# Kernel tuning notes

Measured on AMD Instinct MI355X. Metric: run time of the kernel, lower is better.

## Reference

```python
import jax, jax.numpy as jnp
import numpy as np

D_MODEL = 768
N_HEADS = 4
N_POINTS = 4
PATCH = 16
IMG = 224
HF = IMG // PATCH  # 14
WF = IMG // PATCH  # 14
LQ = HF * WF       # 196 tokens
DH = D_MODEL // N_HEADS  # 192


def setup_inputs() -> dict:
    key = jax.random.key(0)
    ks = jax.random.split(key, 14)
    s = 0.02
    inp = {
        "x": jax.random.normal(ks[0], (4, 16, 3, IMG, IMG), dtype=jnp.float32),
        # patch-embed conv (Conv2d 3->768, k=16, s=16)
        "embed_w": s * jax.random.normal(ks[1], (D_MODEL, 3, PATCH, PATCH), dtype=jnp.float32),
        "embed_b": jnp.zeros((D_MODEL,), dtype=jnp.float32),
        # MSDeformAttn linears (nn.Linear stores W as [out, in]; y = x @ W.T + b)
        "value_w": s * jax.random.normal(ks[2], (D_MODEL, D_MODEL), dtype=jnp.float32),
        "value_b": jnp.zeros((D_MODEL,), dtype=jnp.float32),
        "off_w": s * jax.random.normal(ks[3], (N_HEADS * N_POINTS * 2, D_MODEL), dtype=jnp.float32),
        "off_b": s * jax.random.normal(ks[4], (N_HEADS * N_POINTS * 2,), dtype=jnp.float32),
        "aw_w": s * jax.random.normal(ks[5], (N_HEADS * N_POINTS, D_MODEL), dtype=jnp.float32),
        "aw_b": jnp.zeros((N_HEADS * N_POINTS,), dtype=jnp.float32),
        "outp_w": s * jax.random.normal(ks[6], (D_MODEL, D_MODEL), dtype=jnp.float32),
        "outp_b": jnp.zeros((D_MODEL,), dtype=jnp.float32),
        # final nn.Linear proj
        "proj_w": s * jax.random.normal(ks[7], (D_MODEL, D_MODEL), dtype=jnp.float32),
        "proj_b": jnp.zeros((D_MODEL,), dtype=jnp.float32),
    }
    return inp


def _patch_embed(x, w, b):
    # x: (N,3,H,W); non-overlapping 16x16 patches == Conv2d(3,D,16,16)
    N = x.shape[0]
    xh = x.reshape(N, 3, HF, PATCH, WF, PATCH)
    feat = jnp.einsum('nchpwq,dcpq->nhwd', xh, w) + b  # (N,HF,WF,D)
    return feat.reshape(N, LQ, D_MODEL)


def _ref_points():
    lin = jnp.linspace(0.0, 1.0, HF)
    gy, gx = jnp.meshgrid(lin, lin, indexing='ij')
    return jnp.stack([gx, gy], -1).reshape(LQ, 2)  # (Lq, 2) in [0,1], (x,y)


def _deform_attn_core(value, loc, attn):
    # value: (N, Lq, M, Dh); loc: (N, Lq, M, P, 2) normalized [0,1]; attn: (N, Lq, M, P)
    N = value.shape[0]
    # grid_sample align_corners=False: pixel = (2*loc-1 + 1)*S/2 - 0.5 = loc*S - 0.5
    px = loc[..., 0] * WF - 0.5
    py = loc[..., 1] * HF - 0.5
    x0 = jnp.floor(px).astype(jnp.int32)
    y0 = jnp.floor(py).astype(jnp.int32)
    x1, y1 = x0 + 1, y0 + 1
    wx1 = px - x0.astype(px.dtype)
    wy1 = py - y0.astype(py.dtype)
    wx0, wy0 = 1.0 - wx1, 1.0 - wy1

    valh = value.transpose(0, 2, 1, 3)  # (N, M, HW, Dh)

    def gather(ix, iy):
        valid = (ix >= 0) & (ix < WF) & (iy >= 0) & (iy < HF)  # zeros padding
        idx = jnp.clip(iy, 0, HF - 1) * WF + jnp.clip(ix, 0, WF - 1)
        idxm = idx.transpose(0, 2, 1, 3).reshape(N, N_HEADS, LQ * N_POINTS)
        g = jnp.take_along_axis(valh, idxm[..., None], axis=2)  # (N,M,Lq*P,Dh)
        g = g * valid.transpose(0, 2, 1, 3).reshape(N, N_HEADS, LQ * N_POINTS, 1)
        return g.reshape(N, N_HEADS, LQ, N_POINTS, DH)

    def w4(a, b):  # (N,Lq,M,P) -> (N,M,Lq,P,1)
        return (a * b).transpose(0, 2, 1, 3)[..., None]

    sampled = (w4(wx0, wy0) * gather(x0, y0) + w4(wx1, wy0) * gather(x1, y0)
               + w4(wx0, wy1) * gather(x0, y1) + w4(wx1, wy1) * gather(x1, y1))
    # weighted combine over points
    out = (sampled * attn.transpose(0, 2, 1, 3)[..., None]).sum(3)  # (N,M,Lq,Dh)
    return out.transpose(0, 2, 1, 3).reshape(N, LQ, D_MODEL)


def reference(x, embed_w, embed_b, value_w, value_b, off_w, off_b, aw_w, aw_b,
              outp_w, outp_b, proj_w, proj_b):
    B, T = x.shape[0], x.shape[1]
    N = B * T
    xi = x.reshape(N, 3, IMG, IMG)
    feat = _patch_embed(xi, embed_w, embed_b)  # (N, Lq, D)

    # MSDeformAttn (n_levels=1)
    value = (feat @ value_w.T + value_b).reshape(N, LQ, N_HEADS, DH)
    off = (feat @ off_w.T + off_b).reshape(N, LQ, N_HEADS, N_POINTS, 2)
    aw = (feat @ aw_w.T + aw_b).reshape(N, LQ, N_HEADS, N_POINTS)
    aw = jax.nn.softmax(aw, axis=-1)  # softmax over n_levels*n_points = 4

    ref = _ref_points()  # (Lq, 2)
    norm = jnp.array([WF, HF], dtype=feat.dtype)  # offset_normalizer = (W, H)
    loc = ref[None, :, None, None, :] + off / norm  # (N,Lq,M,P,2)

    out = _deform_attn_core(value, loc, aw)
    out = out @ outp_w.T + outp_b  # output_proj

    pooled = out.mean(axis=1)  # mean over tokens
    final = pooled @ proj_w.T + proj_b
    return final.reshape(B, T, D_MODEL)
```

## Files before the change

kernel.cpp:

```cpp
#include <hip/hip_runtime.h>
#include <hip/hip_bf16.h>


using bf16 = __bf16;
typedef bf16  bf16x8 __attribute__((ext_vector_type(8)));
typedef float f32x4  __attribute__((ext_vector_type(4)));

#define N_IMG   64
#define LQ      196
#define DM      768
#define NH      4
#define DH      192
#define M_ROWS  (N_IMG * LQ)
#define NCAT    896

#define OFF_A      ((size_t)0)
#define OFF_WEMBT  (OFF_A     + 19267584)
#define OFF_WCAT   (OFF_WEMBT + 1179648)
#define OFF_WFUSE  (OFF_WCAT  + 1376256)
#define OFF_BFUSE  (OFF_WFUSE + 1376256)
#define OFF_ZB     (OFF_BFUSE + 4096)
#define OFF_VBUF   (OFF_ZB    + 4096)
#define OFF_OA     (OFF_VBUF  + 19267584)
#define OFF_CORE   (OFF_OA    + 3211264)
#define OFF_POOL   (OFF_CORE  + 196608)

__device__ __forceinline__ void gload_lds16(const bf16* g, bf16* l) {
#if __has_builtin(__builtin_amdgcn_global_load_lds)
  __builtin_amdgcn_global_load_lds(
      (const __attribute__((address_space(1))) void*)g,
      (__attribute__((address_space(3))) void*)l, 16, 0, 0);
#else
  *(bf16x8*)l = *(const bf16x8*)g;
#endif
}

__global__ void stage_kernel(const float* __restrict__ x,
                             const float* __restrict__ embed_w,
                             const float* __restrict__ embed_b,
                             const float* __restrict__ value_w,
                             const float* __restrict__ off_w,
                             const float* __restrict__ aw_w,
                             const float* __restrict__ value_b,
                             const float* __restrict__ off_b,
                             const float* __restrict__ aw_b,
                             bf16* __restrict__ A,
                             bf16* __restrict__ WembT, bf16* __restrict__ Wcat,
                             float* __restrict__ bfused, float* __restrict__ zb,
                             float* __restrict__ core) {
  const int bid = blockIdx.x;
  if (bid < 9408) {
    const int t   = bid * 256 + threadIdx.x;
    const int row = t / 192;
    const int j   = t - row * 192;
    const int k   = j * 4;
    const int c   = k >> 8;
    const int r   = k & 255;
    const int p   = r >> 4;
    const int q   = r & 15;
    const int n   = row / 196;
    const int lq  = row - n * 196;
    const int h   = lq / 14;
    const int w   = lq - h * 14;
    const float4 v = *(const float4*)(x +
        ((((size_t)n * 3 + c) * 224) + h * 16 + p) * 224 + w * 16 + q);
    bf16* dst = A + (size_t)row * DM + k;
    dst[0] = (bf16)v.x; dst[1] = (bf16)v.y; dst[2] = (bf16)v.z; dst[3] = (bf16)v.w;
    return;
  }
  if (bid < 12096) {
    const int idx = (bid - 9408) * 256 + threadIdx.x;
    {
      int rr = idx / DM, kk = idx - rr * DM;
      float v = 0.f;
      if (rr < 768)       v = value_w[idx];
      else if (rr < 800)  v = off_w[(rr - 768) * DM + kk];
      else if (rr < 816)  v = aw_w[(rr - 800) * DM + kk];
      Wcat[idx] = (bf16)v;
    }
    if (idx < DM * DM) {
      int kk = idx / DM, jj = idx - kk * DM;
      WembT[idx] = (bf16)embed_w[(size_t)jj * DM + kk];
    }
    if (idx < DM) zb[idx] = 0.f;
    if (idx < N_IMG * DM) core[idx] = 0.f;
    return;
  }
  const int t  = threadIdx.x;
  const int r  = (bid - 12096) * 32 + (t >> 3);
  const int t8 = t & 7;
  const float* src = nullptr;
  float badd = 0.f;
  if (r < 768)      { src = value_w + (size_t)r * DM;        badd = value_b[r]; }
  else if (r < 800) { src = off_w  + (size_t)(r - 768) * DM; badd = off_b[r - 768]; }
  else if (r < 816) { src = aw_w   + (size_t)(r - 800) * DM; badd = aw_b[r - 800]; }
  float s = 0.f;
  if (src) {
    for (int j = t8; j < DM; j += 8) s += src[j] * embed_b[j];
  }
#pragma unroll
  for (int o = 4; o >= 1; o >>= 1) s += __shfl_down(s, o, 8);
  if (t8 == 0) bfused[r] = (src ? s + badd : 0.f);
}

template <typename OutT>
__global__ void gemm_bt(const bf16* __restrict__ A, const bf16* __restrict__ B,
                        const float* __restrict__ bias, OutT* __restrict__ C,
                        int M, int N, int K) {
  __shared__ bf16 As[128 * 64];
  __shared__ bf16 Bs[128 * 64];

  const int tid  = threadIdx.x;
  const int wave = tid >> 6;
  const int lane = tid & 63;
  const int nBase = blockIdx.x * 128;
  const int mBase = blockIdx.y * 128;
  const int wm = wave & 1;
  const int wn = wave >> 1;
  const int quad = lane >> 4;
  const int r16  = lane & 15;

  const f32x4 zero = {0.f, 0.f, 0.f, 0.f};
  f32x4 acc[4][4];
#pragma unroll
  for (int mi = 0; mi < 4; ++mi)
#pragma unroll
    for (int ni = 0; ni < 4; ++ni) acc[mi][ni] = zero;

  const int srow = wave * 32 + (lane >> 3);
  const int scol = (lane & 7) * 8;
  const bf16* Ag = A + (size_t)(mBase + srow) * K + scol;
  const bf16* Bg = B + (size_t)(nBase + srow) * K + scol;
  bf16* Al = As + srow * 64 + scol;
  bf16* Bl = Bs + srow * 64 + scol;

  for (int kt = 0; kt < K; kt += 64) {
#pragma unroll
    for (int i = 0; i < 4; ++i) {
      gload_lds16(Ag + (size_t)(i * 8) * K + kt, Al + i * 8 * 64);
      gload_lds16(Bg + (size_t)(i * 8) * K + kt, Bl + i * 8 * 64);
    }
    __syncthreads();
#pragma unroll
    for (int kk = 0; kk < 64; kk += 32) {
      bf16x8 af[4], bfr[4];
#pragma unroll
      for (int mi = 0; mi < 4; ++mi)
        af[mi] = *(const bf16x8*)&As[(wm * 64 + mi * 16 + r16) * 64 + kk + quad * 8];
#pragma unroll
      for (int ni = 0; ni < 4; ++ni)
        bfr[ni] = *(const bf16x8*)&Bs[(wn * 64 + ni * 16 + r16) * 64 + kk + quad * 8];
#pragma unroll
      for (int mi = 0; mi < 4; ++mi)
#pragma unroll
        for (int ni = 0; ni < 4; ++ni)
          acc[mi][ni] = __builtin_amdgcn_mfma_f32_16x16x32_bf16(
              af[mi], bfr[ni], acc[mi][ni], 0, 0, 0);
    }
    __syncthreads();
  }

#pragma unroll
  for (int ni = 0; ni < 4; ++ni) {
    const int col = nBase + wn * 64 + ni * 16 + r16;
    const float bv = bias[col];
#pragma unroll
    for (int mi = 0; mi < 4; ++mi) {
      const int row0 = mBase + wm * 64 + mi * 16 + quad * 4;
#pragma unroll
      for (int rr = 0; rr < 4; ++rr) {
        float v = acc[mi][ni][rr] + bv;
        C[(size_t)(row0 + rr) * N + col] = (OutT)v;
      }
    }
  }
}

__global__ void gemm2_mixed(const bf16* __restrict__ A, const bf16* __restrict__ B,
                            const float* __restrict__ bias,
                            bf16* __restrict__ Vb, float* __restrict__ OA,
                            int M, int N, int K) {
  __shared__ bf16 As[128 * 64];
  __shared__ bf16 Bs[128 * 64];

  const int tid  = threadIdx.x;
  const int wave = tid >> 6;
  const int lane = tid & 63;
  const int nBase = blockIdx.x * 128;
  const int mBase = blockIdx.y * 128;
  const int wm = wave & 1;
  const int wn = wave >> 1;
  const int quad = lane >> 4;
  const int r16  = lane & 15;

  const f32x4 zero = {0.f, 0.f, 0.f, 0.f};
  f32x4 acc[4][4];
#pragma unroll
  for (int mi = 0; mi < 4; ++mi)
#pragma unroll
    for (int ni = 0; ni < 4; ++ni) acc[mi][ni] = zero;

  const int srow = wave * 32 + (lane >> 3);
  const int scol = (lane & 7) * 8;
  const bf16* Ag = A + (size_t)(mBase + srow) * K + scol;
  const bf16* Bg = B + (size_t)(nBase + srow) * K + scol;
  bf16* Al = As + srow * 64 + scol;
  bf16* Bl = Bs + srow * 64 + scol;

  for (int kt = 0; kt < K; kt += 64) {
#pragma unroll
    for (int i = 0; i < 4; ++i) {
      gload_lds16(Ag + (size_t)(i * 8) * K + kt, Al + i * 8 * 64);
      gload_lds16(Bg + (size_t)(i * 8) * K + kt, Bl + i * 8 * 64);
    }
    __syncthreads();
#pragma unroll
    for (int kk = 0; kk < 64; kk += 32) {
      bf16x8 af[4], bfr[4];
#pragma unroll
      for (int mi = 0; mi < 4; ++mi)
        af[mi] = *(const bf16x8*)&As[(wm * 64 + mi * 16 + r16) * 64 + kk + quad * 8];
#pragma unroll
      for (int ni = 0; ni < 4; ++ni)
        bfr[ni] = *(const bf16x8*)&Bs[(wn * 64 + ni * 16 + r16) * 64 + kk + quad * 8];
#pragma unroll
      for (int mi = 0; mi < 4; ++mi)
#pragma unroll
        for (int ni = 0; ni < 4; ++ni)
          acc[mi][ni] = __builtin_amdgcn_mfma_f32_16x16x32_bf16(
              af[mi], bfr[ni], acc[mi][ni], 0, 0, 0);
    }
    __syncthreads();
  }

#pragma unroll
  for (int ni = 0; ni < 4; ++ni) {
    const int col = nBase + wn * 64 + ni * 16 + r16;
    const float bv = bias[col];
#pragma unroll
    for (int mi = 0; mi < 4; ++mi) {
      const int row0 = mBase + wm * 64 + mi * 16 + quad * 4;
#pragma unroll
      for (int rr = 0; rr < 4; ++rr) {
        float v = acc[mi][ni][rr] + bv;
        int row = row0 + rr;
        if (col < 768) {
          Vb[(size_t)row * 768 + col] = (bf16)v;
        } else if (col < 816) {
          OA[(size_t)row * 64 + (col - 768)] = v;
        }
      }
    }
  }
}

__global__ void deform_kernel(const bf16* __restrict__ Vb,
                              const float* __restrict__ OA,
                              float* __restrict__ core) {
  __shared__ float s_w[64][4];
  __shared__ int   s_t[64][4];

  const int n   = blockIdx.x;
  const int lq0 = blockIdx.y * 4;
  const int z   = blockIdx.z;
  const int tid = threadIdx.x;

  if (tid < 64) {
    const int i = tid >> 4;
    const int m = (tid >> 2) & 3;
    const int p = tid & 3;
    const int lq = lq0 + i;
    const float* row = OA + ((size_t)n * LQ + lq) * 64;

    const float l0 = row[32 + m * 4 + 0];
    const float l1 = row[32 + m * 4 + 1];
    const float l2 = row[32 + m * 4 + 2];
    const float l3 = row[32 + m * 4 + 3];
    const float mx = fmaxf(fmaxf(l0, l1), fmaxf(l2, l3));
    const float e0 = __expf(l0 - mx), e1 = __expf(l1 - mx);
    const float e2 = __expf(l2 - mx), e3 = __expf(l3 - mx);
    const float inv = 1.f / (e0 + e1 + e2 + e3);
    const float ep[4] = {e0, e1, e2, e3};
    const float ew = ep[p] * inv;

    const int h = lq / 14, w = lq - (lq / 14) * 14;
    const float px = (float)w * (14.f / 13.f) - 0.5f + row[(m * 4 + p) * 2 + 0];
    const float py = (float)h * (14.f / 13.f) - 0.5f + row[(m * 4 + p) * 2 + 1];
    const float fx = floorf(px), fy = floorf(py);
    const int x0 = (int)fx, y0 = (int)fy;
    const float wx1 = px - fx, wy1 = py - fy;
    const float wx0 = 1.f - wx1, wy0 = 1.f - wy1;

    const bool vx0 = (x0 >= 0) & (x0 < 14);
    const bool vx1 = (x0 >= -1) & (x0 < 13);
    const bool vy0 = (y0 >= 0) & (y0 < 14);
    const bool vy1 = (y0 >= -1) & (y0 < 13);
    const int cx0 = min(max(x0, 0), 13),      cx1 = min(max(x0 + 1, 0), 13);
    const int cy0 = min(max(y0, 0), 13) * 14, cy1 = min(max(y0 + 1, 0), 13) * 14;

    s_w[tid][0] = (vx0 & vy0) ? ew * wx0 * wy0 : 0.f;
    s_w[tid][1] = (vx1 & vy0) ? ew * wx1 * wy0 : 0.f;
    s_w[tid][2] = (vx0 & vy1) ? ew * wx0 * wy1 : 0.f;
    s_w[tid][3] = (vx1 & vy1) ? ew * wx1 * wy1 : 0.f;
    s_t[tid][0] = cy0 + cx0;
    s_t[tid][1] = cy0 + cx1;
    s_t[tid][2] = cy1 + cx0;
    s_t[tid][3] = cy1 + cx1;
  }
  __syncthreads();

  const int ch = z * 256 + tid;
  const int m  = ch / DH;
  const bf16* vb = Vb + (size_t)n * LQ * 768 + ch;
  float acc = 0.f;
#pragma unroll
  for (int i = 0; i < 4; ++i) {
#pragma unroll
    for (int p = 0; p < 4; ++p) {
      const int e = i * 16 + m * 4 + p;
      const float4 w4 = *(const float4*)s_w[e];
      const int4   t4 = *(const int4*)s_t[e];
      acc += w4.x * (float)vb[(size_t)t4.x * 768];
      acc += w4.y * (float)vb[(size_t)t4.y * 768];
      acc += w4.z * (float)vb[(size_t)t4.z * 768];
      acc += w4.w * (float)vb[(size_t)t4.w * 768];
    }
  }
  atomicAdd(&core[(size_t)n * DM + ch], acc * (1.f / 196.f));
}

__global__ void small_linear(const float* __restrict__ in,
                             const float* __restrict__ W,
                             const float* __restrict__ b,
                             float* __restrict__ out) {
  const int n = blockIdx.x;
  const int d = blockIdx.y * 256 + threadIdx.x;
  const float4* a4 = (const float4*)(in + (size_t)n * DM);
  const float4* w4 = (const float4*)(W + (size_t)d * DM);
  float acc = 0.f;
#pragma unroll 4
  for (int k = 0; k < DM / 4; ++k) {
    float4 a = a4[k], w = w4[k];
    acc += a.x * w.x + a.y * w.y + a.z * w.z + a.w * w.w;
  }
  out[(size_t)n * DM + d] = acc + b[d];
}

extern "C" void kernel_launch(void* const* d_in, const int* in_sizes, int n_in,
                              void* d_out, int out_size, void* d_ws, size_t ws_size,
                              hipStream_t stream) {
  const float* x       = (const float*)d_in[0];
  const float* embed_w = (const float*)d_in[1];
  const float* embed_b = (const float*)d_in[2];
  const float* value_w = (const float*)d_in[3];
  const float* value_b = (const float*)d_in[4];
  const float* off_w   = (const float*)d_in[5];
  const float* off_b   = (const float*)d_in[6];
  const float* aw_w    = (const float*)d_in[7];
  const float* aw_b    = (const float*)d_in[8];
  const float* outp_w  = (const float*)d_in[9];
  const float* outp_b  = (const float*)d_in[10];
  const float* proj_w  = (const float*)d_in[11];
  const float* proj_b  = (const float*)d_in[12];
  float* out = (float*)d_out;

  char* ws = (char*)d_ws;
  bf16*  A      = (bf16*)(ws + OFF_A);
  bf16*  WembT  = (bf16*)(ws + OFF_WEMBT);
  bf16*  Wcat   = (bf16*)(ws + OFF_WCAT);
  bf16*  Wfused = (bf16*)(ws + OFF_WFUSE);
  float* bfused = (float*)(ws + OFF_BFUSE);
  float* zb     = (float*)(ws + OFF_ZB);
  bf16*  Vbuf   = (bf16*)(ws + OFF_VBUF);
  float* OA     = (float*)(ws + OFF_OA);
  float* core   = (float*)(ws + OFF_CORE);
  float* pooled = (float*)(ws + OFF_POOL);

  stage_kernel<<<dim3(12124), dim3(256), 0, stream>>>(
      x, embed_w, embed_b, value_w, off_w, aw_w, value_b, off_b, aw_b,
      A, WembT, Wcat, bfused, zb, core);

  gemm_bt<bf16><<<dim3(DM / 128, NCAT / 128), dim3(256), 0, stream>>>(
      Wcat, WembT, zb, Wfused, NCAT, DM, DM);

  gemm2_mixed<<<dim3(NCAT / 128, M_ROWS / 128), dim3(256), 0, stream>>>(
      A, Wfused, bfused, Vbuf, OA, M_ROWS, NCAT, DM);

  deform_kernel<<<dim3(N_IMG, 49, 3), dim3(256), 0, stream>>>(Vbuf, OA, core);

  small_linear<<<dim3(N_IMG, 3), dim3(256), 0, stream>>>(core, outp_w, outp_b, pooled);
  small_linear<<<dim3(N_IMG, 3), dim3(256), 0, stream>>>(pooled, proj_w, proj_b, out);
}
```

Measured before the change: 247.9 us.

## Pool sampling weights per token before value projection to skip full value GEMM

Since the output is mean-pooled over tokens and everything downstream is linear, the bilinear sampling weights are accumulated into a per-token coefficient for each image and head. Those coefficients then contract the patch activations, followed by one small matvec with the fused value weights. This removes the large value-projection GEMM and the 19MB value buffer; the GEMM now only computes the 64 offset/attention columns. The small linears are also batched over 16 images per block so each weight row is reused. The catch is that percore_kernel runs only 256 blocks, each looping serially over 196 tokens, and it uses shared-memory float atomics.

```diff
diff --git a/kernel.cpp b/kernel.cpp
--- a/kernel.cpp
+++ b/kernel.cpp
@@ -20,8 +20,7 @@
 #define OFF_WFUSE  (OFF_WCAT  + 1376256)
 #define OFF_BFUSE  (OFF_WFUSE + 1376256)
 #define OFF_ZB     (OFF_BFUSE + 4096)
-#define OFF_VBUF   (OFF_ZB    + 4096)
-#define OFF_OA     (OFF_VBUF  + 19267584)
+#define OFF_OA     (OFF_ZB    + 4096)
 #define OFF_CORE   (OFF_OA    + 3211264)
 #define OFF_POOL   (OFF_CORE  + 196608)
 
@@ -46,8 +45,7 @@
                              const float* __restrict__ aw_b,
                              bf16* __restrict__ A,
                              bf16* __restrict__ WembT, bf16* __restrict__ Wcat,
-                             float* __restrict__ bfused, float* __restrict__ zb,
-                             float* __restrict__ core) {
+                             float* __restrict__ bfused, float* __restrict__ zb) {
   const int bid = blockIdx.x;
   if (bid < 9408) {
     const int t   = bid * 256 + threadIdx.x;
@@ -83,7 +81,6 @@
       WembT[idx] = (bf16)embed_w[(size_t)jj * DM + kk];
     }
     if (idx < DM) zb[idx] = 0.f;
-    if (idx < N_IMG * DM) core[idx] = 0.f;
     return;
   }
   const int t  = threadIdx.x;
@@ -103,9 +100,8 @@
   if (t8 == 0) bfused[r] = (src ? s + badd : 0.f);
 }
 
-template <typename OutT>
 __global__ void gemm_bt(const bf16* __restrict__ A, const bf16* __restrict__ B,
-                        const float* __restrict__ bias, OutT* __restrict__ C,
+                        const float* __restrict__ bias, bf16* __restrict__ C,
                         int M, int N, int K) {
   __shared__ bf16 As[128 * 64];
   __shared__ bf16 Bs[128 * 64];
@@ -169,25 +165,22 @@
       const int row0 = mBase + wm * 64 + mi * 16 + quad * 4;
 #pragma unroll
       for (int rr = 0; rr < 4; ++rr) {
-        float v = acc[mi][ni][rr] + bv;
-        C[(size_t)(row0 + rr) * N + col] = (OutT)v;
+        C[(size_t)(row0 + rr) * N + col] = (bf16)(acc[mi][ni][rr] + bv);
       }
     }
   }
 }
 
-__global__ void gemm2_mixed(const bf16* __restrict__ A, const bf16* __restrict__ B,
-                            const float* __restrict__ bias,
-                            bf16* __restrict__ Vb, float* __restrict__ OA,
-                            int M, int N, int K) {
+__global__ void gemm_oa(const bf16* __restrict__ A, const bf16* __restrict__ B,
+                        const float* __restrict__ bias, float* __restrict__ OA,
+                        int K) {
   __shared__ bf16 As[128 * 64];
   __shared__ bf16 Bs[128 * 64];
 
   const int tid  = threadIdx.x;
   const int wave = tid >> 6;
   const int lane = tid & 63;
-  const int nBase = blockIdx.x * 128;
-  const int mBase = blockIdx.y * 128;
+  const int mBase = blockIdx.x * 128;
   const int wm = wave & 1;
   const int wn = wave >> 1;
   const int quad = lane >> 4;
@@ -203,7 +196,7 @@
   const int srow = wave * 32 + (lane >> 3);
   const int scol = (lane & 7) * 8;
   const bf16* Ag = A + (size_t)(mBase + srow) * K + scol;
-  const bf16* Bg = B + (size_t)(nBase + srow) * K + scol;
+  const bf16* Bg = B + (size_t)srow * K + scol;
   bf16* Al = As + srow * 64 + scol;
   bf16* Bl = Bs + srow * 64 + scol;
 
@@ -235,43 +228,41 @@
 
 #pragma unroll
   for (int ni = 0; ni < 4; ++ni) {
-    const int col = nBase + wn * 64 + ni * 16 + r16;
+    const int col = wn * 64 + ni * 16 + r16;
+    if (col >= 64) continue;
     const float bv = bias[col];
 #pragma unroll
     for (int mi = 0; mi < 4; ++mi) {
       const int row0 = mBase + wm * 64 + mi * 16 + quad * 4;
 #pragma unroll
       for (int rr = 0; rr < 4; ++rr) {
-        float v = acc[mi][ni][rr] + bv;
-        int row = row0 + rr;
-        if (col < 768) {
-          Vb[(size_t)row * 768 + col] = (bf16)v;
-        } else if (col < 816) {
-          OA[(size_t)row * 64 + (col - 768)] = v;
-        }
+        OA[(size_t)(row0 + rr) * 64 + col] = acc[mi][ni][rr] + bv;
       }
     }
   }
 }
 
-__global__ void deform_kernel(const bf16* __restrict__ Vb,
-                              const float* __restrict__ OA,
-                              float* __restrict__ core) {
-  __shared__ float s_w[64][4];
-  __shared__ int   s_t[64][4];
-
-  const int n   = blockIdx.x;
-  const int lq0 = blockIdx.y * 4;
-  const int z   = blockIdx.z;
+__global__ void percore_kernel(const bf16* __restrict__ A,
+                               const float* __restrict__ OA,
+                               const bf16* __restrict__ Wfused,
+                               const float* __restrict__ bfused,
+                               float* __restrict__ core) {
+  __shared__ float sC[LQ];
+  __shared__ float sS[DM];
+  __shared__ float sSum;
+
+  const int n = blockIdx.x;
+  const int m = blockIdx.y;
   const int tid = threadIdx.x;
 
-  if (tid < 64) {
-    const int i = tid >> 4;
-    const int m = (tid >> 2) & 3;
-    const int p = tid & 3;
-    const int lq = lq0 + i;
-    const float* row = OA + ((size_t)n * LQ + lq) * 64;
-
+  if (tid < LQ) sC[tid] = 0.f;
+  if (tid == 0) sSum = 0.f;
+  __syncthreads();
+
+  const float* oa = OA + (size_t)n * LQ * 64;
+  for (int t = tid; t < LQ * 4; t += 256) {
+    const int lq = t >> 2, p = t & 3;
+    const float* row = oa + (size_t)lq * 64;
     const float l0 = row[32 + m * 4 + 0];
     const float l1 = row[32 + m * 4 + 1];
     const float l2 = row[32 + m * 4 + 2];
@@ -298,52 +289,64 @@
     const int cx0 = min(max(x0, 0), 13),      cx1 = min(max(x0 + 1, 0), 13);
     const int cy0 = min(max(y0, 0), 13) * 14, cy1 = min(max(y0 + 1, 0), 13) * 14;
 
-    s_w[tid][0] = (vx0 & vy0) ? ew * wx0 * wy0 : 0.f;
-    s_w[tid][1] = (vx1 & vy0) ? ew * wx1 * wy0 : 0.f;
-    s_w[tid][2] = (vx0 & vy1) ? ew * wx0 * wy1 : 0.f;
-    s_w[tid][3] = (vx1 & vy1) ? ew * wx1 * wy1 : 0.f;
-    s_t[tid][0] = cy0 + cx0;
-    s_t[tid][1] = cy0 + cx1;
-    s_t[tid][2] = cy1 + cx0;
-    s_t[tid][3] = cy1 + cx1;
+    atomicAdd(&sC[cy0 + cx0], (vx0 & vy0) ? ew * wx0 * wy0 : 0.f);
+    atomicAdd(&sC[cy0 + cx1], (vx1 & vy0) ? ew * wx1 * wy0 : 0.f);
+    atomicAdd(&sC[cy1 + cx0], (vx0 & vy1) ? ew * wx0 * wy1 : 0.f);
+    atomicAdd(&sC[cy1 + cx1], (vx1 & vy1) ? ew * wx1 * wy1 : 0.f);
   }
   __syncthreads();
-
-  const int ch = z * 256 + tid;
-  const int m  = ch / DH;
-  const bf16* vb = Vb + (size_t)n * LQ * 768 + ch;
-  float acc = 0.f;
-#pragma unroll
-  for (int i = 0; i < 4; ++i) {
-#pragma unroll
-    for (int p = 0; p < 4; ++p) {
-      const int e = i * 16 + m * 4 + p;
-      const float4 w4 = *(const float4*)s_w[e];
-      const int4   t4 = *(const int4*)s_t[e];
-      acc += w4.x * (float)vb[(size_t)t4.x * 768];
-      acc += w4.y * (float)vb[(size_t)t4.y * 768];
-      acc += w4.z * (float)vb[(size_t)t4.z * 768];
-      acc += w4.w * (float)vb[(size_t)t4.w * 768];
-    }
-  }
-  atomicAdd(&core[(size_t)n * DM + ch], acc * (1.f / 196.f));
-}
-
-__global__ void small_linear(const float* __restrict__ in,
-                             const float* __restrict__ W,
-                             const float* __restrict__ b,
-                             float* __restrict__ out) {
-  const int n = blockIdx.x;
-  const int d = blockIdx.y * 256 + threadIdx.x;
-  const float4* a4 = (const float4*)(in + (size_t)n * DM);
+  if (tid < LQ) atomicAdd(&sSum, sC[tid]);
+  __syncthreads();
+
+  {
+    const bf16* an = A + (size_t)n * LQ * DM;
+    float a0 = 0.f, a1 = 0.f, a2 = 0.f;
+    const int c0 = tid, c1 = tid + 256, c2 = tid + 512;
+    for (int tok = 0; tok < LQ; ++tok) {
+      const float cf = sC[tok];
+      const bf16* ar = an + (size_t)tok * DM;
+      a0 += cf * (float)ar[c0];
+      a1 += cf * (float)ar[c1];
+      a2 += cf * (float)ar[c2];
+    }
+    sS[c0] = a0; sS[c1] = a1; sS[c2] = a2;
+  }
+  __syncthreads();
+
+  if (tid < DH) {
+    const int ch = m * DH + tid;
+    const bf16* wr = Wfused + (size_t)ch * DM;
+    float acc = 0.f;
+    for (int k = 0; k < DM; k += 8) {
+      const bf16x8 wv = *(const bf16x8*)(wr + k);
+#pragma unroll
+      for (int j = 0; j < 8; ++j) acc += (float)wv[j] * sS[k + j];
+    }
+    core[(size_t)n * DM + ch] = (acc + sSum * bfused[ch]) * (1.f / 196.f);
+  }
+}
+
+__global__ void small_linear_b(const float* __restrict__ in,
+                               const float* __restrict__ W,
+                               const float* __restrict__ b,
+                               float* __restrict__ out) {
+  const int d  = blockIdx.x * 256 + threadIdx.x;
+  const int n0 = blockIdx.y * 16;
   const float4* w4 = (const float4*)(W + (size_t)d * DM);
-  float acc = 0.f;
-#pragma unroll 4
+  float acc[16];
+#pragma unroll
+  for (int j = 0; j < 16; ++j) acc[j] = 0.f;
   for (int k = 0; k < DM / 4; ++k) {
-    float4 a = a4[k], w = w4[k];
-    acc += a.x * w.x + a.y * w.y + a.z * w.z + a.w * w.w;
-  }
-  out[(size_t)n * DM + d] = acc + b[d];
+    const float4 w = w4[k];
+#pragma unroll
+    for (int j = 0; j < 16; ++j) {
+      const float4 a = *(const float4*)(in + (size_t)(n0 + j) * DM + k * 4);
+      acc[j] += a.x * w.x + a.y * w.y + a.z * w.z + a.w * w.w;
+    }
+  }
+  const float bv = b[d];
+#pragma unroll
+  for (int j = 0; j < 16; ++j) out[(size_t)(n0 + j) * DM + d] = acc[j] + bv;
 }
 
 extern "C" void kernel_launch(void* const* d_in, const int* in_sizes, int n_in,
@@ -371,23 +374,23 @@
   bf16*  Wfused = (bf16*)(ws + OFF_WFUSE);
   float* bfused = (float*)(ws + OFF_BFUSE);
   float* zb     = (float*)(ws + OFF_ZB);
-  bf16*  Vbuf   = (bf16*)(ws + OFF_VBUF);
   float* OA     = (float*)(ws + OFF_OA);
   float* core   = (float*)(ws + OFF_CORE);
   float* pooled = (float*)(ws + OFF_POOL);
 
   stage_kernel<<<dim3(12124), dim3(256), 0, stream>>>(
       x, embed_w, embed_b, value_w, off_w, aw_w, value_b, off_b, aw_b,
-      A, WembT, Wcat, bfused, zb, core);
-
-  gemm_bt<bf16><<<dim3(DM / 128, NCAT / 128), dim3(256), 0, stream>>>(
+      A, WembT, Wcat, bfused, zb);
+
+  gemm_bt<<<dim3(DM / 128, NCAT / 128), dim3(256), 0, stream>>>(
       Wcat, WembT, zb, Wfused, NCAT, DM, DM);
 
-  gemm2_mixed<<<dim3(NCAT / 128, M_ROWS / 128), dim3(256), 0, stream>>>(
-      A, Wfused, bfused, Vbuf, OA, M_ROWS, NCAT, DM);
-
-  deform_kernel<<<dim3(N_IMG, 49, 3), dim3(256), 0, stream>>>(Vbuf, OA, core);
-
-  small_linear<<<dim3(N_IMG, 3), dim3(256), 0, stream>>>(core, outp_w, outp_b, pooled);
-  small_linear<<<dim3(N_IMG, 3), dim3(256), 0, stream>>>(pooled, proj_w, proj_b, out);
-}
+  gemm_oa<<<dim3(M_ROWS / 128), dim3(256), 0, stream>>>(
+      A, Wfused + (size_t)768 * DM, bfused + 768, OA, DM);
+
+  percore_kernel<<<dim3(N_IMG, NH), dim3(256), 0, stream>>>(
+      A, OA, Wfused, bfused, core);
+
+  small_linear_b<<<dim3(3, 4), dim3(256), 0, stream>>>(core, outp_w, outp_b, pooled);
+  small_linear_b<<<dim3(3, 4), dim3(256), 0, stream>>>(pooled, proj_w, proj_b, out);
+}
```

Result: slower. 354.8 us (+43.1%).
